# Optimization experiments

Hardware: AMD Instinct MI355X
Metric: run time of the kernel (lower is better)

The kernel has to match this reference:

```python
import jax, jax.numpy as jnp
import numpy as np

N_HEADS, N_KV, HEAD_DIM, D_MODEL, T_MAX = 16, 4, 64, 1024, 2048
GROUPS = N_HEADS // N_KV
EPS = 1e-6


def _rms_norm(x, w):
    # RMSNorm over last dim (head_dim), computed in fp32 like the torch module
    xf = x.astype(jnp.float32)
    r = jax.lax.rsqrt(jnp.mean(xf * xf, axis=-1, keepdims=True) + EPS)
    return (xf * r).astype(x.dtype) * w


def _apply_rope(x, cos, sin):
    # x: (B, H, T, D); cos/sin: (T_max, D/2)
    T = x.shape[2]
    c = cos[:T][None, None]  # (1,1,T,D/2)
    s = sin[:T][None, None]
    x1, x2 = jnp.split(x, 2, axis=-1)
    return jnp.concatenate([x1 * c - x2 * s, x2 * c + x1 * s], axis=-1)


def setup_inputs() -> dict:
    key = jax.random.key(0)
    ks = jax.random.split(key, 8)
    B, T = 2, 2048
    x = jax.random.normal(ks[0], (B, T, D_MODEL), dtype=jnp.float32)
    # realistic RoPE tables
    theta = 10000.0
    inv_freq = 1.0 / (theta ** (np.arange(0, HEAD_DIM, 2, dtype=np.float32) / HEAD_DIM))
    t = np.arange(T_MAX, dtype=np.float32)
    freqs = np.outer(t, inv_freq)  # (T_max, D/2)
    cos = jnp.asarray(np.cos(freqs))
    sin = jnp.asarray(np.sin(freqs))
    sd = 0.02
    wq = jax.random.normal(ks[1], (N_HEADS * HEAD_DIM, D_MODEL), dtype=jnp.float32) * sd
    wk = jax.random.normal(ks[2], (N_KV * HEAD_DIM, D_MODEL), dtype=jnp.float32) * sd
    wv = jax.random.normal(ks[3], (N_KV * HEAD_DIM, D_MODEL), dtype=jnp.float32) * sd
    wo = jax.random.normal(ks[4], (D_MODEL, N_HEADS * HEAD_DIM), dtype=jnp.float32) * sd
    qn_w = jnp.ones((HEAD_DIM,), dtype=jnp.float32)
    kn_w = jnp.ones((HEAD_DIM,), dtype=jnp.float32)
    return {"x": x, "cos": cos, "sin": sin, "wq": wq, "wk": wk, "wv": wv,
            "wo": wo, "qn_w": qn_w, "kn_w": kn_w}


def reference(x, cos, sin, wq, wk, wv, wo, qn_w, kn_w):
    B, T, _ = x.shape
    scale = HEAD_DIM ** -0.5
    # projections (torch Linear: y = x @ W.T)
    q = (x @ wq.T).reshape(B, T, N_HEADS, HEAD_DIM).transpose(0, 2, 1, 3)
    k = (x @ wk.T).reshape(B, T, N_KV, HEAD_DIM).transpose(0, 2, 1, 3)
    v = (x @ wv.T).reshape(B, T, N_KV, HEAD_DIM).transpose(0, 2, 1, 3)
    # qk RMSNorm
    q = _rms_norm(q, qn_w)
    k = _rms_norm(k, kn_w)
    # RoPE
    q = _apply_rope(q, cos, sin)
    k = _apply_rope(k, cos, sin)
    # GQA expansion: query head h uses kv head h // GROUPS
    k = jnp.repeat(k, GROUPS, axis=1)  # (B, H, T, D)
    v = jnp.repeat(v, GROUPS, axis=1)
    # causal SDPA
    scores = jnp.einsum('bhqd,bhkd->bhqk', q, k) * scale
    causal = jnp.tril(jnp.ones((T, T), dtype=bool))
    scores = jnp.where(causal, scores, jnp.finfo(scores.dtype).min)
    p = jax.nn.softmax(scores, axis=-1)
    out = jnp.einsum('bhqk,bhkd->bhqd', p, v)
    out = out.transpose(0, 2, 1, 3).reshape(B, T, N_HEADS * HEAD_DIM)
    return out @ wo.T
```

## Files before the change

kernel.cpp:

```cpp
#include <hip/hip_runtime.h>


typedef __bf16 bf16;
typedef __attribute__((ext_vector_type(4))) __bf16 bf16x4;
typedef __attribute__((ext_vector_type(8))) __bf16 bf16x8;
typedef __attribute__((ext_vector_type(4))) float f32x4;

#define MFMA(a, b, c) __builtin_amdgcn_mfma_f32_16x16x32_bf16((a), (b), (c), 0, 0, 0)
#define GLOAD_LDS16(g, l)                                        \
  __builtin_amdgcn_global_load_lds(                              \
      (const __attribute__((address_space(1))) void*)(g),        \
      (__attribute__((address_space(3))) void*)(l), 16, 0, 0)

__device__ __forceinline__ bool is_bf16_input(const void* cosRaw) {
  return ((const unsigned short*)cosRaw)[0] == 0x3F80;
}
__device__ __forceinline__ float rdval(const void* p, int idx, bool isbf) {
  return isbf ? (float)((const bf16*)p)[idx] : ((const float*)p)[idx];
}

__global__ __launch_bounds__(256) void convert_kernel(
    const void* __restrict__ x, const void* __restrict__ wq,
    const void* __restrict__ wk, const void* __restrict__ wv,
    const void* __restrict__ wo, bf16* __restrict__ dx,
    bf16* __restrict__ dw, const void* __restrict__ cosraw) {
  const bool isbf = is_bf16_input(cosraw);
  const int c = (int)blockIdx.x * 256 + (int)threadIdx.x;
  const void* src;
  int off;
  bf16* dst;
  int dc;
  if (c < 524288)      { src = x;  off = c;          dst = dx; dc = c; }
  else if (c < 655360) { src = wq; off = c - 524288; dst = dw; dc = c - 524288; }
  else if (c < 688128) { src = wk; off = c - 655360; dst = dw; dc = c - 524288; }
  else if (c < 720896) { src = wv; off = c - 688128; dst = dw; dc = c - 524288; }
  else                 { src = wo; off = c - 720896; dst = dw; dc = c - 524288; }
  bf16x8 o;
  if (isbf) {
    o = ((const bf16x8*)src)[off];
  } else {
    const float4* fp = (const float4*)src + (size_t)off * 2;
    float4 f0 = fp[0];
    float4 f1 = fp[1];
    o[0] = (bf16)f0.x; o[1] = (bf16)f0.y; o[2] = (bf16)f0.z; o[3] = (bf16)f0.w;
    o[4] = (bf16)f1.x; o[5] = (bf16)f1.y; o[6] = (bf16)f1.z; o[7] = (bf16)f1.w;
  }
  ((bf16x8*)dst)[dc] = o;
}

__global__ __launch_bounds__(256, 3) void proj_kernel(
    const bf16* __restrict__ xb, const bf16* __restrict__ wqb,
    const bf16* __restrict__ wkb, const bf16* __restrict__ wvb,
    bf16* __restrict__ qp, bf16* __restrict__ kp, bf16* __restrict__ vt,
    const void* __restrict__ cosraw, const void* __restrict__ sinraw,
    const void* __restrict__ qnraw, const void* __restrict__ knraw) {
  __shared__ bf16 As[128 * 64];
  __shared__ bf16 Bs[64 * 64];

  const int idx = (int)blockIdx.x;
  const int xcd = idx & 7;
  const int jj = idx >> 3;
  const int mb = (jj & 3) * 8 + xcd;
  const int nb = jj >> 2;
  const int n0 = nb * 64;
  const int m0 = mb * 128;

  const int tid = threadIdx.x;
  const int wave = tid >> 6;
  const int lane = tid & 63;
  const int q16 = lane & 15;
  const int quad = lane >> 4;
  const int srow = lane >> 3;
  const int csrc = (lane & 7) ^ srow;
  const int x7 = q16 & 7;

  const bf16* wsrc;
  int nr0;
  if (nb < 16)      { wsrc = wqb; nr0 = n0; }
  else if (nb < 20) { wsrc = wkb; nr0 = n0 - 1024; }
  else              { wsrc = wvb; nr0 = n0 - 1280; }

  f32x4 acc[2][4];
#pragma unroll
  for (int mf = 0; mf < 2; ++mf)
#pragma unroll
    for (int nt = 0; nt < 4; ++nt) acc[mf][nt] = (f32x4){0.f, 0.f, 0.f, 0.f};

  for (int kt = 0; kt < 16; ++kt) {
    const int ko = kt * 64;
#pragma unroll
    for (int i = 0; i < 4; ++i) {
      int rb = wave * 32 + i * 8;
      GLOAD_LDS16(&xb[(size_t)(m0 + rb + srow) * 1024 + ko + csrc * 8],
                  &As[rb * 64]);
    }
#pragma unroll
    for (int i = 0; i < 2; ++i) {
      int rb = wave * 16 + i * 8;
      GLOAD_LDS16(&wsrc[(size_t)(nr0 + rb + srow) * 1024 + ko + csrc * 8],
                  &Bs[rb * 64]);
    }
    __syncthreads();

    bf16x8 a[2][2], bfr[4][2];
#pragma unroll
    for (int mf = 0; mf < 2; ++mf) {
      const bf16* rp = &As[(wave * 32 + mf * 16 + q16) * 64];
      a[mf][0] = *(const bf16x8*)&rp[(quad ^ x7) * 8];
      a[mf][1] = *(const bf16x8*)&rp[((quad + 4) ^ x7) * 8];
    }
#pragma unroll
    for (int nt = 0; nt < 4; ++nt) {
      const bf16* rp = &Bs[(nt * 16 + q16) * 64];
      bfr[nt][0] = *(const bf16x8*)&rp[(quad ^ x7) * 8];
      bfr[nt][1] = *(const bf16x8*)&rp[((quad + 4) ^ x7) * 8];
    }
#pragma unroll
    for (int nt = 0; nt < 4; ++nt)
#pragma unroll
      for (int mf = 0; mf < 2; ++mf) {
        acc[mf][nt] = MFMA(a[mf][0], bfr[nt][0], acc[mf][nt]);
        acc[mf][nt] = MFMA(a[mf][1], bfr[nt][1], acc[mf][nt]);
      }
    __syncthreads();
  }

  if (nb < 20) {
    const bool isbf = is_bf16_input(cosraw);
    const void* nwp = (nb < 16) ? qnraw : knraw;
    const float osc = (nb < 16) ? 0.18033688f : 1.0f;
    float wd[4];
#pragma unroll
    for (int nt = 0; nt < 4; ++nt) wd[nt] = rdval(nwp, nt * 16 + q16, isbf);

#pragma unroll
    for (int mf = 0; mf < 2; ++mf) {
#pragma unroll
      for (int r = 0; r < 4; ++r) {
        float p = acc[mf][0][r] * acc[mf][0][r] + acc[mf][1][r] * acc[mf][1][r] +
                  acc[mf][2][r] * acc[mf][2][r] + acc[mf][3][r] * acc[mf][3][r];
#pragma unroll
        for (int off = 8; off >= 1; off >>= 1) p += __shfl_xor(p, off);
        float rms = rsqrtf(p * (1.0f / 64.0f) + 1e-6f);

        int row = m0 + wave * 32 + mf * 16 + quad * 4 + r;
        int t = row & 2047;
        float c0 = rdval(cosraw, t * 32 + q16, isbf);
        float c1 = rdval(cosraw, t * 32 + 16 + q16, isbf);
        float s0 = rdval(sinraw, t * 32 + q16, isbf);
        float s1 = rdval(sinraw, t * 32 + 16 + q16, isbf);

        float v0 = acc[mf][0][r] * rms * wd[0];
        float v1 = acc[mf][1][r] * rms * wd[1];
        float v2 = acc[mf][2][r] * rms * wd[2];
        float v3 = acc[mf][3][r] * rms * wd[3];

        bf16* op = (nb < 16) ? &qp[(size_t)row * 1024 + nb * 64]
                             : &kp[(size_t)row * 256 + (nb - 16) * 64];
        op[0 * 16 + q16] = (bf16)((v0 * c0 - v2 * s0) * osc);
        op[1 * 16 + q16] = (bf16)((v1 * c1 - v3 * s1) * osc);
        op[2 * 16 + q16] = (bf16)((v2 * c0 + v0 * s0) * osc);
        op[3 * 16 + q16] = (bf16)((v3 * c1 + v1 * s1) * osc);
      }
    }
  } else {
    const int vh = nb - 20;
    const int b = m0 >> 11;
    const int tbase = m0 & 2047;
#pragma unroll
    for (int mf = 0; mf < 2; ++mf)
#pragma unroll
      for (int nt = 0; nt < 4; ++nt)
#pragma unroll
        for (int r = 0; r < 4; ++r)
          As[(wave * 32 + mf * 16 + quad * 4 + r) * 64 + nt * 16 + q16] =
              (bf16)acc[mf][nt][r];
    __syncthreads();
#pragma unroll
    for (int rep = 0; rep < 4; ++rep) {
      int c = tid + 256 * rep;
      int d = c >> 4;
      int t8 = (c & 15) * 8;
      bf16x8 pk;
#pragma unroll
      for (int j = 0; j < 8; ++j) pk[j] = As[(t8 + j) * 64 + d];
      *(bf16x8*)&vt[(((size_t)(b * 4 + vh)) * 64 + d) * 2048 + tbase + t8] = pk;
    }
  }
}

__global__ __launch_bounds__(256, 4) void flash_kernel(
    const bf16* __restrict__ qp, const bf16* __restrict__ kp,
    const bf16* __restrict__ vt, bf16* __restrict__ attn) {
  const int qblk = blockIdx.z ? 31 - (int)blockIdx.x : (int)blockIdx.x;
  const int h = blockIdx.y;
  const int b = blockIdx.z;
  const int kvh = h >> 2;
  const int tid = threadIdx.x;
  const int wave = tid >> 6;
  const int lane = tid & 63;
  const int q16 = lane & 15;
  const int quad = lane >> 4;
  const int r7 = q16 & 7;
  const int t0 = qblk * 64 + wave * 16;

  __shared__ bf16 Ks[2][64 * 64];
  __shared__ bf16 Vs[2][64 * 64];
  __shared__ bf16 Pl[4][16 * 32];

  const bf16* qrow = qp + (((size_t)(b * 2048 + t0 + q16)) * 16 + h) * 64;
  bf16x8 qa0 = *(const bf16x8*)(qrow + quad * 8);
  bf16x8 qa1 = *(const bf16x8*)(qrow + 32 + quad * 8);

  bf16x8 ones;
#pragma unroll
  for (int j = 0; j < 8; ++j) ones[j] = (bf16)1.0f;

  f32x4 O[4], l4;
#pragma unroll
  for (int nt = 0; nt < 4; ++nt) O[nt] = (f32x4){0.f, 0.f, 0.f, 0.f};
  l4 = (f32x4){0.f, 0.f, 0.f, 0.f};

  const int ntile = qblk + 1;

  bf16x8 kr[2], vr[2];
  const int cr = tid * 2;
  const int krow = cr >> 3;
  const size_t kgbase = (((size_t)(b * 2048) + krow) * 4 + kvh) * 64;
  const size_t vgbase = ((size_t)(b * 4 + kvh) * 64 + krow) * 2048;

  auto gload = [&](int tk) {
#pragma unroll
    for (int rep = 0; rep < 2; ++rep) {
      int ch = (cr + rep) & 7;
      kr[rep] = *(const bf16x8*)&kp[kgbase + (size_t)(tk * 64) * 256 + ch * 8];
      vr[rep] = *(const bf16x8*)&vt[vgbase + tk * 64 + ch * 8];
    }
  };
  auto swrite = [&](int bb) {
#pragma unroll
    for (int rep = 0; rep < 2; ++rep) {
      int ch = (cr + rep) & 7;
      int pos = (ch ^ (krow & 7)) * 8;
      *(bf16x8*)&Ks[bb][krow * 64 + pos] = kr[rep];
      *(bf16x8*)&Vs[bb][krow * 64 + pos] = vr[rep];
    }
  };

  gload(0);

  for (int t = 0; t < ntile; ++t) {
    const int bb = t & 1;
    const int kbase = t * 64;
    swrite(bb);
    __syncthreads();
    if (t + 1 < ntile) gload(t + 1);

    f32x4 s[4];
    __builtin_amdgcn_s_setprio(1);
#pragma unroll
    for (int kt = 0; kt < 4; ++kt) {
      const bf16* kr0 = &Ks[bb][(kt * 16 + q16) * 64];
      bf16x8 kb0 = *(const bf16x8*)&kr0[(quad ^ r7) * 8];
      bf16x8 kb1 = *(const bf16x8*)&kr0[((quad + 4) ^ r7) * 8];
      f32x4 z = (f32x4){0.f, 0.f, 0.f, 0.f};
      z = MFMA(kb0, qa0, z);
      z = MFMA(kb1, qa1, z);
      s[kt] = z;
    }
    __builtin_amdgcn_s_setprio(0);

    if (kbase + 63 > t0) {
      const int q = t0 + q16;
#pragma unroll
      for (int kt = 0; kt < 4; ++kt) {
        int jt = kbase + kt * 16 + quad * 4;
#pragma unroll
        for (int r = 0; r < 4; ++r)
          if (jt + r > q) s[kt][r] = -1e30f;
      }
    }

#pragma unroll
    for (int kt = 0; kt < 4; ++kt)
#pragma unroll
      for (int r = 0; r < 4; ++r) s[kt][r] = exp2f(s[kt][r] - 12.98425007f);

#pragma unroll
    for (int kh = 0; kh < 2; ++kh) {
#pragma unroll
      for (int ct = 0; ct < 2; ++ct) {
        const int kt = kh * 2 + ct;
        bf16x4 pk;
#pragma unroll
        for (int r = 0; r < 4; ++r) pk[r] = (bf16)s[kt][r];
        *(bf16x4*)&Pl[wave][q16 * 32 + ((ct * 4 + quad) ^ (q16 & 6)) * 4] = pk;
      }
      bf16x8 pa = *(const bf16x8*)&Pl[wave][q16 * 32 + ((quad * 2) ^ (q16 & 6)) * 4];
      __builtin_amdgcn_s_setprio(1);
#pragma unroll
      for (int nt = 0; nt < 4; ++nt) {
        const bf16* vr0 = &Vs[bb][(nt * 16 + q16) * 64];
        bf16x8 vb = *(const bf16x8*)&vr0[((kh * 4 + quad) ^ r7) * 8];
        O[nt] = MFMA(pa, vb, O[nt]);
      }
      l4 = MFMA(pa, ones, l4);
      __builtin_amdgcn_s_setprio(0);
    }
  }

  float inv[4];
#pragma unroll
  for (int r = 0; r < 4; ++r) inv[r] = 1.0f / l4[r];
#pragma unroll
  for (int nt = 0; nt < 4; ++nt)
#pragma unroll
    for (int r = 0; r < 4; ++r) {
      size_t o = (((size_t)(b * 2048 + t0 + quad * 4 + r)) * 16 + h) * 64 +
                 nt * 16 + q16;
      attn[o] = (bf16)(O[nt][r] * inv[r]);
    }
}

__global__ __launch_bounds__(256, 6) void gemm_o_kernel(
    const bf16* __restrict__ A, const bf16* __restrict__ W,
    void* __restrict__ C, const void* __restrict__ cosraw) {
  __shared__ bf16 As[64 * 64];
  __shared__ bf16 Bs[64 * 64];

  const int idx = (int)blockIdx.x;
  const int xcd = idx & 7;
  const int jj = idx >> 3;
  const int mb = (jj & 7) * 8 + xcd;
  const int nb = jj >> 3;
  const int n0 = nb * 64;
  const int m0 = mb * 64;

  const int tid = threadIdx.x;
  const int wave = tid >> 6;
  const int lane = tid & 63;
  const int q16 = lane & 15;
  const int quad = lane >> 4;
  const int srow = lane >> 3;
  const int csrc = (lane & 7) ^ srow;
  const int wm = wave * 16;
  const int x7 = q16 & 7;
  const bool isbf = is_bf16_input(cosraw);

  f32x4 acc[4];
#pragma unroll
  for (int nt = 0; nt < 4; ++nt) acc[nt] = (f32x4){0.f, 0.f, 0.f, 0.f};

  for (int kt = 0; kt < 16; ++kt) {
    const int ko = kt * 64;
#pragma unroll
    for (int i = 0; i < 2; ++i) {
      int rb = wave * 16 + i * 8;
      GLOAD_LDS16(&A[(size_t)(m0 + rb + srow) * 1024 + ko + csrc * 8],
                  &As[rb * 64]);
      GLOAD_LDS16(&W[(size_t)(n0 + rb + srow) * 1024 + ko + csrc * 8],
                  &Bs[rb * 64]);
    }
    __syncthreads();

    bf16x8 a0, a1, bfr[4][2];
    {
      const bf16* rp = &As[(wm + q16) * 64];
      a0 = *(const bf16x8*)&rp[(quad ^ x7) * 8];
      a1 = *(const bf16x8*)&rp[((quad + 4) ^ x7) * 8];
    }
#pragma unroll
    for (int nt = 0; nt < 4; ++nt) {
      const bf16* rp = &Bs[(nt * 16 + q16) * 64];
      bfr[nt][0] = *(const bf16x8*)&rp[(quad ^ x7) * 8];
      bfr[nt][1] = *(const bf16x8*)&rp[((quad + 4) ^ x7) * 8];
    }
#pragma unroll
    for (int nt = 0; nt < 4; ++nt) {
      acc[nt] = MFMA(a0, bfr[nt][0], acc[nt]);
      acc[nt] = MFMA(a1, bfr[nt][1], acc[nt]);
    }
    __syncthreads();
  }

#pragma unroll
  for (int nt = 0; nt < 4; ++nt)
#pragma unroll
    for (int r = 0; r < 4; ++r) {
      size_t idx2 = (size_t)(m0 + wm + quad * 4 + r) * 1024 + n0 + nt * 16 + q16;
      if (isbf) ((bf16*)C)[idx2] = (bf16)acc[nt][r];
      else      ((float*)C)[idx2] = acc[nt][r];
    }
}

extern "C" void kernel_launch(void* const* d_in, const int* in_sizes, int n_in,
                              void* d_out, int out_size, void* d_ws, size_t ws_size,
                              hipStream_t stream) {
  bf16* qp = (bf16*)d_ws;
  bf16* kp = qp + (size_t)4194304;
  bf16* vt = kp + (size_t)1048576;
  bf16* at = vt + (size_t)1048576;
  bf16* xb = at + (size_t)4194304;
  bf16* dw = xb + (size_t)4194304;

  bf16* wqb = dw;
  bf16* wkb = dw + (size_t)1048576;
  bf16* wvb = dw + (size_t)1310720;
  bf16* wob = dw + (size_t)1572864;

  convert_kernel<<<3328, 256, 0, stream>>>(
      d_in[0], d_in[3], d_in[4], d_in[5], d_in[6], xb, dw, d_in[1]);

  proj_kernel<<<768, 256, 0, stream>>>(
      xb, wqb, wkb, wvb, qp, kp, vt,
      d_in[1], d_in[2], d_in[7], d_in[8]);

  flash_kernel<<<dim3(32, 16, 2), 256, 0, stream>>>(qp, kp, vt, at);

  gemm_o_kernel<<<1024, 256, 0, stream>>>(at, wob, d_out, d_in[1]);
}
```

Baseline: 162.2 us.

## Read K and V tiles directly from global memory in flash kernel

Removes the LDS double-buffered K/V staging, the cooperative loads and the per-tile block barrier from the flash attention kernel. Each wave now loads its MFMA operands for K and V straight from global memory, relying on L1/L2 to serve the reuse across the four waves. With LDS use cut to the small P buffer, the occupancy hint is raised to 6 blocks per CU, and the s_setprio hints are dropped. The cost is redundant global/cache traffic (each wave rereads the same K/V tile) and exposed load latency with no explicit prefetch.

Measured after the change: 266.3 us. +64.2%, slower.

```diff
diff --git a/kernel.cpp b/kernel.cpp
--- a/kernel.cpp
+++ b/kernel.cpp
@@ -189,7 +189,7 @@
   }
 }
 
-__global__ __launch_bounds__(256, 4) void flash_kernel(
+__global__ __launch_bounds__(256, 6) void flash_kernel(
     const bf16* __restrict__ qp, const bf16* __restrict__ kp,
     const bf16* __restrict__ vt, bf16* __restrict__ attn) {
   const int qblk = blockIdx.z ? 31 - (int)blockIdx.x : (int)blockIdx.x;
@@ -201,17 +201,17 @@
   const int lane = tid & 63;
   const int q16 = lane & 15;
   const int quad = lane >> 4;
-  const int r7 = q16 & 7;
   const int t0 = qblk * 64 + wave * 16;
 
-  __shared__ bf16 Ks[2][64 * 64];
-  __shared__ bf16 Vs[2][64 * 64];
   __shared__ bf16 Pl[4][16 * 32];
 
   const bf16* qrow = qp + (((size_t)(b * 2048 + t0 + q16)) * 16 + h) * 64;
   bf16x8 qa0 = *(const bf16x8*)(qrow + quad * 8);
   bf16x8 qa1 = *(const bf16x8*)(qrow + 32 + quad * 8);
 
+  const bf16* kptr = kp + (((size_t)(b * 2048 + q16)) * 4 + kvh) * 64 + quad * 8;
+  const bf16* vptr = vt + ((size_t)(b * 4 + kvh) * 64 + q16) * 2048 + quad * 8;
+
   bf16x8 ones;
 #pragma unroll
   for (int j = 0; j < 8; ++j) ones[j] = (bf16)1.0f;
@@ -223,52 +223,20 @@
 
   const int ntile = qblk + 1;
 
-  bf16x8 kr[2], vr[2];
-  const int cr = tid * 2;
-  const int krow = cr >> 3;
-  const size_t kgbase = (((size_t)(b * 2048) + krow) * 4 + kvh) * 64;
-  const size_t vgbase = ((size_t)(b * 4 + kvh) * 64 + krow) * 2048;
-
-  auto gload = [&](int tk) {
-#pragma unroll
-    for (int rep = 0; rep < 2; ++rep) {
-      int ch = (cr + rep) & 7;
-      kr[rep] = *(const bf16x8*)&kp[kgbase + (size_t)(tk * 64) * 256 + ch * 8];
-      vr[rep] = *(const bf16x8*)&vt[vgbase + tk * 64 + ch * 8];
-    }
-  };
-  auto swrite = [&](int bb) {
-#pragma unroll
-    for (int rep = 0; rep < 2; ++rep) {
-      int ch = (cr + rep) & 7;
-      int pos = (ch ^ (krow & 7)) * 8;
-      *(bf16x8*)&Ks[bb][krow * 64 + pos] = kr[rep];
-      *(bf16x8*)&Vs[bb][krow * 64 + pos] = vr[rep];
-    }
-  };
-
-  gload(0);
-
   for (int t = 0; t < ntile; ++t) {
-    const int bb = t & 1;
     const int kbase = t * 64;
-    swrite(bb);
-    __syncthreads();
-    if (t + 1 < ntile) gload(t + 1);
 
     f32x4 s[4];
-    __builtin_amdgcn_s_setprio(1);
 #pragma unroll
     for (int kt = 0; kt < 4; ++kt) {
-      const bf16* kr0 = &Ks[bb][(kt * 16 + q16) * 64];
-      bf16x8 kb0 = *(const bf16x8*)&kr0[(quad ^ r7) * 8];
-      bf16x8 kb1 = *(const bf16x8*)&kr0[((quad + 4) ^ r7) * 8];
+      const bf16* kr0 = kptr + (size_t)(kbase + kt * 16) * 256;
+      bf16x8 kb0 = *(const bf16x8*)kr0;
+      bf16x8 kb1 = *(const bf16x8*)(kr0 + 32);
       f32x4 z = (f32x4){0.f, 0.f, 0.f, 0.f};
       z = MFMA(kb0, qa0, z);
       z = MFMA(kb1, qa1, z);
       s[kt] = z;
     }
-    __builtin_amdgcn_s_setprio(0);
 
     if (kbase + 63 > t0) {
       const int q = t0 + q16;
@@ -296,16 +264,15 @@
         for (int r = 0; r < 4; ++r) pk[r] = (bf16)s[kt][r];
         *(bf16x4*)&Pl[wave][q16 * 32 + ((ct * 4 + quad) ^ (q16 & 6)) * 4] = pk;
       }
-      bf16x8 pa = *(const bf16x8*)&Pl[wave][q16 * 32 + ((quad * 2) ^ (q16 & 6)) * 4];
-      __builtin_amdgcn_s_setprio(1);
+      bf16x8 pa =
+          *(const bf16x8*)&Pl[wave][q16 * 32 + ((quad * 2) ^ (q16 & 6)) * 4];
 #pragma unroll
       for (int nt = 0; nt < 4; ++nt) {
-        const bf16* vr0 = &Vs[bb][(nt * 16 + q16) * 64];
-        bf16x8 vb = *(const bf16x8*)&vr0[((kh * 4 + quad) ^ r7) * 8];
+        bf16x8 vb = *(const bf16x8*)(vptr + (size_t)(nt * 16) * 2048 + kbase +
+                                     kh * 32);
         O[nt] = MFMA(pa, vb, O[nt]);
       }
       l4 = MFMA(pa, ones, l4);
-      __builtin_amdgcn_s_setprio(0);
     }
   }
 
```
